# Kernel tuning notes

Hardware: AMD Instinct MI355X
Metric: run time of the kernel (lower is better)

## Reference

```python
import jax, jax.numpy as jnp
import numpy as np

EPS_LN = 1e-6


def _ln(x):
    m = jnp.mean(x, axis=-1, keepdims=True)
    v = jnp.mean((x - m) ** 2, axis=-1, keepdims=True)
    return (x - m) * jax.lax.rsqrt(v + EPS_LN)


def _rope(q, cos, sin):
    # q: [B,S,H,D]; cos/sin: [S, D//2]; rotate interleaved pairs
    q2 = q.reshape(q.shape[:-1] + (-1, 2))
    a, b = q2[..., 0], q2[..., 1]
    c = cos[None, :, None, :]
    s = sin[None, :, None, :]
    return jnp.stack([a * c - b * s, a * s + b * c], axis=-1).reshape(q.shape)


def _attn(q, k, v):
    # q:[B,Sq,H,D] k,v:[B,Sk,H,D] -> [B,Sq,H,D]; flash default scale 1/sqrt(D)
    D = q.shape[-1]
    scores = jnp.einsum('bqhd,bkhd->bhqk', q, k) / jnp.sqrt(jnp.asarray(D, q.dtype))
    p = jax.nn.softmax(scores, axis=-1)
    return jnp.einsum('bhqk,bkhd->bqhd', p, v)


def setup_inputs() -> dict:
    key = jax.random.key(0)
    C, H, S, T, B = 2048, 16, 1024, 256, 4
    Dh = C // H
    F = int(C * 4)
    L, Ly = B * S, B * T
    ks = jax.random.split(key, 24)

    def w(k, shape):
        return (jax.random.normal(k, shape, dtype=jnp.float32) * 0.02)

    # RoPE angle table: positions 0..S-1 with standard inverse frequencies
    inv_freq = 1.0 / (10000.0 ** (np.arange(0, Dh, 2, dtype=np.float32) / Dh))
    freqs = jnp.asarray(np.arange(S, dtype=np.float32)[:, None] * inv_freq[None, :])

    inp = {
        'x': jax.random.normal(ks[0], (L, C), dtype=jnp.float32),
        'y': jax.random.normal(ks[1], (Ly, C), dtype=jnp.float32),
        't': jax.random.normal(ks[2], (L, 6 * C), dtype=jnp.float32),
        'freqs': freqs,
        'scale_shift_table': jax.random.normal(ks[3], (6, C), dtype=jnp.float32) / (C ** 0.5),
        'Wq_s': w(ks[4], (C, C)), 'bq_s': jnp.zeros((C,), jnp.float32),
        'Wk_s': w(ks[5], (C, C)), 'bk_s': jnp.zeros((C,), jnp.float32),
        'Wv_s': w(ks[6], (C, C)), 'bv_s': jnp.zeros((C,), jnp.float32),
        'Wo_s': w(ks[7], (C, C)), 'bo_s': jnp.zeros((C,), jnp.float32),
        'Wq_c': w(ks[8], (C, C)), 'bq_c': jnp.zeros((C,), jnp.float32),
        'Wk_c': w(ks[9], (C, C)), 'bk_c': jnp.zeros((C,), jnp.float32),
        'Wv_c': w(ks[10], (C, C)), 'bv_c': jnp.zeros((C,), jnp.float32),
        'Wo_c': w(ks[11], (C, C)), 'bo_c': jnp.zeros((C,), jnp.float32),
        'W_fc1': w(ks[12], (F, C)), 'b_fc1': jnp.zeros((F,), jnp.float32),
        'W_fc2': w(ks[13], (C, F)), 'b_fc2': jnp.zeros((C,), jnp.float32),
        'seq_len': S,
        'txt_len': T,
    }
    return inp


def reference(x, y, t, freqs, scale_shift_table,
              Wq_s, bq_s, Wk_s, bk_s, Wv_s, bv_s, Wo_s, bo_s,
              Wq_c, bq_c, Wk_c, bk_c, Wv_c, bv_c, Wo_c, bo_c,
              W_fc1, b_fc1, W_fc2, b_fc2, seq_len, txt_len):
    L, C = x.shape
    Dh = 2 * freqs.shape[1]
    H = C // Dh
    B = L // seq_len
    cos, sin = jnp.cos(freqs), jnp.sin(freqs)

    # per-token AdaLN params (B here == total tokens in torch code)
    mods = scale_shift_table[None] + t.reshape(L, 6, C)
    shift_msa, scale_msa, gate_msa, shift_mlp, scale_mlp, gate_mlp = (
        mods[:, i, :] for i in range(6))

    # ---- self attention (AdaLN modulate + RoPE) ----
    xm = _ln(x) * (1.0 + scale_msa) + shift_msa
    q = (xm @ Wq_s.T + bq_s).reshape(B, seq_len, H, Dh)
    k = (xm @ Wk_s.T + bk_s).reshape(B, seq_len, H, Dh)
    v = (xm @ Wv_s.T + bv_s).reshape(B, seq_len, H, Dh)
    q = _rope(q, cos, sin)
    k = _rope(k, cos, sin)
    a = _attn(q, k, v).reshape(L, C)
    x = x + gate_msa * (a @ Wo_s.T + bo_s)

    # ---- cross attention (no norm/modulation/gate, no RoPE) ----
    q = (x @ Wq_c.T + bq_c).reshape(B, seq_len, H, Dh)
    k = (y @ Wk_c.T + bk_c).reshape(B, txt_len, H, Dh)
    v = (y @ Wv_c.T + bv_c).reshape(B, txt_len, H, Dh)
    a = _attn(q, k, v).reshape(L, C)
    x = x + (a @ Wo_c.T + bo_c)

    # ---- MLP with AdaLN modulate + gate ----
    xm = _ln(x) * (1.0 + scale_mlp) + shift_mlp
    h = jax.nn.gelu(xm @ W_fc1.T + b_fc1, approximate=True)
    x = x + gate_mlp * (h @ W_fc2.T + b_fc2)
    return x
```

## Files before the change

kernel.cpp:

```cpp
#include <hip/hip_runtime.h>
#include <stdint.h>

#define C_DIM 2048
#define H_NUM 16
#define DH    128
#define S_LEN 1024
#define T_LEN 256
#define B_SZ  4
#define L_ROWS 4096
#define LY_ROWS 1024
#define F_DIM 8192

typedef __attribute__((ext_vector_type(4))) float f32x4;
typedef __attribute__((ext_vector_type(8))) __bf16 bf16x8;
typedef __attribute__((ext_vector_type(4))) unsigned short us4;
typedef __attribute__((ext_vector_type(8))) unsigned short us8;
typedef unsigned short u16;

__device__ __forceinline__ u16 f2bf(float f) {
  union { float f; uint32_t u; } v; v.f = f;
  uint32_t r = v.u + 0x7FFFu + ((v.u >> 16) & 1u);
  return (u16)(r >> 16);
}
__device__ __forceinline__ float bf2f(u16 h) {
  union { uint32_t u; float f; } v; v.u = ((uint32_t)h) << 16;
  return v.f;
}

typedef __attribute__((address_space(1))) void gvoid;
typedef __attribute__((address_space(3))) void lvoid;
__device__ __forceinline__ void gl_lds16(const void* g, void* l) {
  __builtin_amdgcn_global_load_lds((gvoid*)g, (lvoid*)l, 16, 0, 0);
}

template<int N> __device__ __forceinline__ void wait_vmcnt() {
  if constexpr (N == 0) asm volatile("s_waitcnt vmcnt(0)" ::: "memory");
  else if constexpr (N == 5) asm volatile("s_waitcnt vmcnt(5)" ::: "memory");
  else if constexpr (N == 6) asm volatile("s_waitcnt vmcnt(6)" ::: "memory");
}
__device__ __forceinline__ void barrier_raw() {
  asm volatile("s_barrier" ::: "memory");
}
__device__ __forceinline__ void lgkm0_pin() {
  asm volatile("s_waitcnt lgkmcnt(0)" ::: "memory");
  __builtin_amdgcn_sched_barrier(0);
}

__global__ void k_cvt(const float* __restrict__ src, u16* __restrict__ dst, int n) {
  int i = (blockIdx.x * blockDim.x + threadIdx.x) * 4;
  int stride = gridDim.x * blockDim.x * 4;
  for (; i < n; i += stride) {
    float4 v = *(const float4*)(src + i);
    us4 o;
    o[0] = f2bf(v.x); o[1] = f2bf(v.y); o[2] = f2bf(v.z); o[3] = f2bf(v.w);
    *(us4*)(dst + i) = o;
  }
}

__global__ __launch_bounds__(256)
void k_modln(const float* __restrict__ x, const float* __restrict__ t,
             const float* __restrict__ tab, u16* __restrict__ out,
             int scale_idx, int shift_idx) {
  int row = blockIdx.x;
  int tid = threadIdx.x;
  const float* xr = x + (size_t)row * C_DIM;
  int c0 = tid * 8;
  float4 a = *(const float4*)(xr + c0);
  float4 b = *(const float4*)(xr + c0 + 4);
  float v[8] = {a.x, a.y, a.z, a.w, b.x, b.y, b.z, b.w};
  float s = 0.f, ss = 0.f;
#pragma unroll
  for (int j = 0; j < 8; ++j) { s += v[j]; ss += v[j] * v[j]; }
#pragma unroll
  for (int m = 1; m < 64; m <<= 1) { s += __shfl_xor(s, m); ss += __shfl_xor(ss, m); }
  __shared__ float red[8];
  int wid = tid >> 6;
  if ((tid & 63) == 0) { red[wid * 2] = s; red[wid * 2 + 1] = ss; }
  __syncthreads();
  s  = red[0] + red[2] + red[4] + red[6];
  ss = red[1] + red[3] + red[5] + red[7];
  float mean = s * (1.f / C_DIM);
  float var  = ss * (1.f / C_DIM) - mean * mean;
  float rstd = rsqrtf(var + 1e-6f);
  const float* trow = t + (size_t)row * (6 * C_DIM);
  const float* tsc = trow + scale_idx * C_DIM + c0;
  const float* tsh = trow + shift_idx * C_DIM + c0;
  const float* gsc = tab + scale_idx * C_DIM + c0;
  const float* gsh = tab + shift_idx * C_DIM + c0;
  us8 o;
#pragma unroll
  for (int j = 0; j < 8; ++j) {
    float scv = 1.f + gsc[j] + tsc[j];
    float shv = gsh[j] + tsh[j];
    o[j] = f2bf((v[j] - mean) * rstd * scv + shv);
  }
  *(us8*)(out + (size_t)row * C_DIM + c0) = o;
}

template<int BM, int EPI>
__global__ __launch_bounds__(512, 2)
void k_gemm3(const u16* __restrict__ A, const u16* __restrict__ W,
             const float* __restrict__ bias0, const float* __restrict__ bias1,
             const float* __restrict__ bias2,
             u16* __restrict__ o0, u16* __restrict__ o1, u16* __restrict__ o2,
             int sec_shift, int out_ld,
             float* __restrict__ outF, const float* __restrict__ resid,
             const float* __restrict__ gate_t, const float* __restrict__ gate_tab,
             const float* __restrict__ partial,
             int M, int N, int K, int lda, int ldw, int nbx) {
  constexpr int HTA = (BM / 2) * 64;
  constexpr int HTB = 128 * 64;
  constexpr int ACALLS = BM / 128;
  constexpr int QM = BM / 64;
  constexpr int MFR = BM / 32;
  constexpr int VMN = 4 + ACALLS;
  constexpr int BOFF = 4 * HTA;
  __shared__ __align__(16) u16 lds[BOFF + 4 * HTB];

  int tid = threadIdx.x;
  int nwg = gridDim.x;
  int q8 = nwg >> 3, r8 = nwg & 7;
  int xcd = blockIdx.x & 7, local = blockIdx.x >> 3;
  int wgid = (xcd < r8 ? xcd * (q8 + 1) : r8 * (q8 + 1) + (xcd - r8) * q8) + local;
  int bx = wgid % nbx, by = wgid / nbx;
  int m0 = by * BM, n0 = bx * 256;

  int wid = tid >> 6, lane = tid & 63;
  int wm = wid >> 2, wn = wid & 3;
  int lr = lane & 15, lg = lane >> 4;
  int xorslot = lr & 7;
  int bcol = (wn & 1) * 64;

  int srow = tid >> 3;
  int scol = ((tid ^ (tid >> 3)) & 7) * 8;

  auto stA = [&](int h, int kt2) {
    int pt = kt2 & 1;
    u16* dst = lds + (pt * 2 + h) * HTA + tid * 8;
#pragma unroll
    for (int call = 0; call < ACALLS; ++call) {
      int grow = m0 + h * (BM / 2) + call * 64 + srow;
      gl_lds16(A + (size_t)grow * lda + kt2 * 64 + scol, dst + call * 4096);
    }
  };
  auto stB = [&](int h, int kt2) {
    int pt = kt2 & 1;
    u16* dst = lds + BOFF + (pt * 2 + h) * HTB + tid * 8;
#pragma unroll
    for (int call = 0; call < 2; ++call) {
      int grow = n0 + h * 128 + call * 64 + srow;
      gl_lds16(W + (size_t)grow * ldw + kt2 * 64 + scol, dst + call * 4096);
    }
  };

  f32x4 zero4 = {0.f, 0.f, 0.f, 0.f};
  f32x4 acc[MFR][4];
#pragma unroll
  for (int m = 0; m < MFR; ++m)
#pragma unroll
    for (int n = 0; n < 4; ++n) acc[m][n] = zero4;

  int NT2 = K >> 6;
  stA(0, 0); stA(1, 0); stB(0, 0); stB(1, 0);
  stB(0, 1); stB(1, 1); stA(0, 1);
  wait_vmcnt<VMN>();
  barrier_raw();

  for (int kt = 0; kt < NT2; ++kt) {
    int p = kt & 1;
    const u16* Ah = lds + (p * 2 + wm) * HTA;
    const u16* Bh = lds + BOFF + (p * 2 + (wn >> 1)) * HTB;
    bf16x8 aR[QM][2], bR0[2][2], bR1[2][2];
    bool st1 = (kt + 1) < NT2, st2 = (kt + 2) < NT2;

#pragma unroll
    for (int m = 0; m < QM; ++m) {
      int r = m * 16 + lr;
#pragma unroll
      for (int kk = 0; kk < 2; ++kk)
        aR[m][kk] = *(const bf16x8*)(Ah + r * 64 + ((((kk << 2) | lg) ^ xorslot)) * 8);
    }
#pragma unroll
    for (int n = 0; n < 2; ++n) {
      int r = bcol + n * 16 + lr;
#pragma unroll
      for (int kk = 0; kk < 2; ++kk)
        bR0[n][kk] = *(const bf16x8*)(Bh + r * 64 + ((((kk << 2) | lg) ^ xorslot)) * 8);
    }
    if (st1) stA(1, kt + 1);
    lgkm0_pin();
    __builtin_amdgcn_s_setprio(1);
#pragma unroll
    for (int kk = 0; kk < 2; ++kk)
#pragma unroll
      for (int m = 0; m < QM; ++m)
#pragma unroll
        for (int n = 0; n < 2; ++n)
          acc[m][n] = __builtin_amdgcn_mfma_f32_16x16x32_bf16(aR[m][kk], bR0[n][kk], acc[m][n], 0, 0, 0);
    __builtin_amdgcn_s_setprio(0);
    barrier_raw();

#pragma unroll
    for (int n = 0; n < 2; ++n) {
      int r = bcol + 32 + n * 16 + lr;
#pragma unroll
      for (int kk = 0; kk < 2; ++kk)
        bR1[n][kk] = *(const bf16x8*)(Bh + r * 64 + ((((kk << 2) | lg) ^ xorslot)) * 8);
    }
    lgkm0_pin();
    __builtin_amdgcn_s_setprio(1);
#pragma unroll
    for (int kk = 0; kk < 2; ++kk)
#pragma unroll
      for (int m = 0; m < QM; ++m)
#pragma unroll
        for (int n = 0; n < 2; ++n)
          acc[m][2 + n] = __builtin_amdgcn_mfma_f32_16x16x32_bf16(aR[m][kk], bR1[n][kk], acc[m][2 + n], 0, 0, 0);
    __builtin_amdgcn_s_setprio(0);
    barrier_raw();

#pragma unroll
    for (int m = 0; m < QM; ++m) {
      int r = (BM / 4) + m * 16 + lr;
#pragma unroll
      for (int kk = 0; kk < 2; ++kk)
        aR[m][kk] = *(const bf16x8*)(Ah + r * 64 + ((((kk << 2) | lg) ^ xorslot)) * 8);
    }
    if (st2) { stB(0, kt + 2); stB(1, kt + 2); }
    lgkm0_pin();
    __builtin_amdgcn_s_setprio(1);
#pragma unroll
    for (int kk = 0; kk < 2; ++kk)
#pragma unroll
      for (int m = 0; m < QM; ++m)
#pragma unroll
        for (int n = 0; n < 2; ++n)
          acc[QM + m][2 + n] = __builtin_amdgcn_mfma_f32_16x16x32_bf16(aR[m][kk], bR1[n][kk], acc[QM + m][2 + n], 0, 0, 0);
    __builtin_amdgcn_s_setprio(0);
    barrier_raw();

    if (st2) stA(0, kt + 2);
    __builtin_amdgcn_s_setprio(1);
#pragma unroll
    for (int kk = 0; kk < 2; ++kk)
#pragma unroll
      for (int m = 0; m < QM; ++m)
#pragma unroll
        for (int n = 0; n < 2; ++n)
          acc[QM + m][n] = __builtin_amdgcn_mfma_f32_16x16x32_bf16(aR[m][kk], bR0[n][kk], acc[QM + m][n], 0, 0, 0);
    __builtin_amdgcn_s_setprio(0);
    if (st2) wait_vmcnt<VMN>(); else wait_vmcnt<0>();
    barrier_raw();
  }

#pragma unroll
  for (int mf = 0; mf < MFR; ++mf) {
    int row0 = m0 + wm * (BM / 2) + mf * 16 + lg * 4;
#pragma unroll
    for (int nf = 0; nf < 4; ++nf) {
      int col = n0 + wn * 64 + nf * 16 + lr;
      if constexpr (EPI == 0) {
        int sec = col >> sec_shift;
        const float* bp = sec == 0 ? bias0 : (sec == 1 ? bias1 : bias2);
        u16* op = sec == 0 ? o0 : (sec == 1 ? o1 : o2);
        int cs = col & ((1 << sec_shift) - 1);
        float bv = bp[cs];
#pragma unroll
        for (int r = 0; r < 4; ++r)
          op[(size_t)(row0 + r) * out_ld + cs] = f2bf(acc[mf][nf][r] + bv);
      } else if constexpr (EPI == 1) {
        float bv = bias0[col];
#pragma unroll
        for (int r = 0; r < 4; ++r) {
          float val = acc[mf][nf][r] + bv;
          float x3 = val * val * val;
          float g = 0.5f * val * (1.f + tanhf(0.7978845608f * (val + 0.044715f * x3)));
          o0[(size_t)(row0 + r) * out_ld + col] = f2bf(g);
        }
      } else if constexpr (EPI == 2) {
        float bv = bias0[col];
        float gt = gate_tab[col];
#pragma unroll
        for (int r = 0; r < 4; ++r) {
          int row = row0 + r;
          size_t idx = (size_t)row * N + col;
          float g = gt + gate_t[(size_t)row * (6 * C_DIM) + col];
          float o = resid[idx] + g * (acc[mf][nf][r] + bv);
          outF[idx] = o;
          if (o0) o0[idx] = f2bf(o);
        }
      } else if constexpr (EPI == 3) {
        float bv = bias0[col];
#pragma unroll
        for (int r = 0; r < 4; ++r) {
          size_t idx = (size_t)(row0 + r) * N + col;
          outF[idx] = resid[idx] + (acc[mf][nf][r] + bv);
        }
      } else if constexpr (EPI == 4) {
#pragma unroll
        for (int r = 0; r < 4; ++r)
          outF[(size_t)(row0 + r) * N + col] = acc[mf][nf][r];
      } else {
        float bv = bias0[col];
        float gt = gate_tab[col];
#pragma unroll
        for (int r = 0; r < 4; ++r) {
          int row = row0 + r;
          size_t idx = (size_t)row * N + col;
          float val = acc[mf][nf][r] + partial[idx] + bv;
          float g = gt + gate_t[(size_t)row * (6 * C_DIM) + col];
          outF[idx] = resid[idx] + g * val;
        }
      }
    }
  }
}

__global__ void k_rope(u16* __restrict__ q, u16* __restrict__ k,
                       const float* __restrict__ freqs) {
  int idx = blockIdx.x * blockDim.x + threadIdx.x;
  int total = L_ROWS * C_DIM / 8;
  for (; idx < total; idx += gridDim.x * blockDim.x) {
    int e = idx * 8;
    int row = e >> 11;
    int col = e & (C_DIM - 1);
    int s = row & (S_LEN - 1);
    int i0 = (col & (DH - 1)) >> 1;
    float4 fr = *(const float4*)(freqs + s * (DH / 2) + i0);
    float cs[4], sn[4];
    float fv[4] = {fr.x, fr.y, fr.z, fr.w};
#pragma unroll
    for (int j = 0; j < 4; ++j) sincosf(fv[j], &sn[j], &cs[j]);
    us8 qa = *(us8*)(q + e);
    us8 ka = *(us8*)(k + e);
#pragma unroll
    for (int p = 0; p < 4; ++p) {
      float a = bf2f(qa[2 * p]), b = bf2f(qa[2 * p + 1]);
      qa[2 * p]     = f2bf(a * cs[p] - b * sn[p]);
      qa[2 * p + 1] = f2bf(a * sn[p] + b * cs[p]);
      float a2 = bf2f(ka[2 * p]), b2 = bf2f(ka[2 * p + 1]);
      ka[2 * p]     = f2bf(a2 * cs[p] - b2 * sn[p]);
      ka[2 * p + 1] = f2bf(a2 * sn[p] + b2 * cs[p]);
    }
    *(us8*)(q + e) = qa;
    *(us8*)(k + e) = ka;
  }
}

__global__ void k_transpose_v(const u16* __restrict__ v, u16* __restrict__ vt, int Lkv) {
  __shared__ u16 tile[32][33];
  int bh = blockIdx.x, b = bh >> 4, h = bh & 15;
  int k0 = blockIdx.y * 32, d0 = blockIdx.z * 32;
  int tx = threadIdx.x, ty = threadIdx.y;
  const u16* src = v + (size_t)(b * Lkv) * C_DIM + h * DH;
#pragma unroll
  for (int j = 0; j < 32; j += 8)
    tile[ty + j][tx] = src[(size_t)(k0 + ty + j) * C_DIM + d0 + tx];
  __syncthreads();
  u16* dst = vt + (size_t)bh * DH * Lkv;
#pragma unroll
  for (int j = 0; j < 32; j += 8)
    dst[(size_t)(d0 + ty + j) * Lkv + k0 + tx] = tile[tx][ty + j];
}

__global__ __launch_bounds__(256)
void k_flash(const u16* __restrict__ Q, const u16* __restrict__ K,
             const u16* __restrict__ Vt, u16* __restrict__ O,
             int Lq, int Lkv, float scale) {
  __shared__ __align__(16) u16 lK[64 * 128];
  __shared__ __align__(16) u16 lV[128 * 64];
  __shared__ __align__(16) u16 lP[4][16 * 72];
  int bh = blockIdx.x, b = bh >> 4, h = bh & 15;
  int tid = threadIdx.x, wid = tid >> 6, lane = tid & 63;
  int lr = lane & 15, lg = lane >> 4;
  int q0 = blockIdx.y * 64 + wid * 16;
  const u16* Qb = Q + ((size_t)(b * Lq) + q0) * C_DIM + h * DH;
  const u16* Kb = K + (size_t)(b * Lkv) * C_DIM + h * DH;
  const u16* Vb = Vt + (size_t)bh * DH * Lkv;

  bf16x8 qf[4];
#pragma unroll
  for (int ks = 0; ks < 4; ++ks)
    qf[ks] = *(const bf16x8*)(Qb + (size_t)lr * C_DIM + ks * 32 + lg * 8);

  f32x4 zero4 = {0.f, 0.f, 0.f, 0.f};
  f32x4 o[8];
#pragma unroll
  for (int n = 0; n < 8; ++n) o[n] = zero4;
  float mrow[4] = {-3.0e38f, -3.0e38f, -3.0e38f, -3.0e38f};
  float lrow[4] = {0.f, 0.f, 0.f, 0.f};

  int nsteps = Lkv >> 6;
  for (int kt = 0; kt < nsteps; ++kt) {
#pragma unroll
    for (int i = 0; i < 4; ++i) {
      int flat = i * 4096 + tid * 16;
      int key = flat >> 8, inner = flat & 255;
      int ksrc = inner ^ ((key & 7) << 4);
      gl_lds16((const char*)Kb + ((size_t)(kt * 64 + key) * C_DIM) * 2 + ksrc, (char*)lK + flat);
      int d = flat >> 7, keyb = flat & 127;
      int vsrc = keyb ^ ((d & 7) << 4);
      gl_lds16((const char*)Vb + ((size_t)d * Lkv) * 2 + kt * 128 + vsrc, (char*)lV + flat);
    }
    __syncthreads();

    f32x4 sc[4];
#pragma unroll
    for (int c = 0; c < 4; ++c) sc[c] = zero4;
#pragma unroll
    for (int c = 0; c < 4; ++c) {
      int key = c * 16 + lr;
#pragma unroll
      for (int ks = 0; ks < 4; ++ks) {
        int off = (ks * 64 + lg * 16) ^ ((key & 7) << 4);
        bf16x8 kf = *(const bf16x8*)((const char*)lK + key * 256 + off);
        sc[c] = __builtin_amdgcn_mfma_f32_16x16x32_bf16(qf[ks], kf, sc[c], 0, 0, 0);
      }
    }
#pragma unroll
    for (int r = 0; r < 4; ++r) {
      float s0 = sc[0][r] * scale, s1 = sc[1][r] * scale;
      float s2 = sc[2][r] * scale, s3 = sc[3][r] * scale;
      float mx = fmaxf(fmaxf(s0, s1), fmaxf(s2, s3));
#pragma unroll
      for (int m = 1; m < 16; m <<= 1) mx = fmaxf(mx, __shfl_xor(mx, m));
      float mnew = fmaxf(mrow[r], mx);
      float alpha = exp2f((mrow[r] - mnew) * 1.44269504f);
      mrow[r] = mnew;
      float p0 = exp2f((s0 - mnew) * 1.44269504f);
      float p1 = exp2f((s1 - mnew) * 1.44269504f);
      float p2 = exp2f((s2 - mnew) * 1.44269504f);
      float p3 = exp2f((s3 - mnew) * 1.44269504f);
      float psum = p0 + p1 + p2 + p3;
#pragma unroll
      for (int m = 1; m < 16; m <<= 1) psum += __shfl_xor(psum, m);
      lrow[r] = lrow[r] * alpha + psum;
#pragma unroll
      for (int n = 0; n < 8; ++n) o[n][r] *= alpha;
      u16* pr = lP[wid] + (4 * lg + r) * 72;
      pr[lr]      = f2bf(p0);
      pr[16 + lr] = f2bf(p1);
      pr[32 + lr] = f2bf(p2);
      pr[48 + lr] = f2bf(p3);
    }
    asm volatile("s_waitcnt lgkmcnt(0)" ::: "memory");
    __builtin_amdgcn_sched_barrier(0);
#pragma unroll
    for (int half = 0; half < 2; ++half) {
      bf16x8 pf = *(const bf16x8*)(lP[wid] + lr * 72 + half * 32 + lg * 8);
#pragma unroll
      for (int n = 0; n < 8; ++n) {
        int d = n * 16 + lr;
        int off = (half * 64 + lg * 16) ^ ((d & 7) << 4);
        bf16x8 vf = *(const bf16x8*)((const char*)lV + d * 128 + off);
        o[n] = __builtin_amdgcn_mfma_f32_16x16x32_bf16(pf, vf, o[n], 0, 0, 0);
      }
    }
    __syncthreads();
  }

  u16* Ob = O + ((size_t)(b * Lq) + q0) * C_DIM + h * DH;
#pragma unroll
  for (int n = 0; n < 8; ++n) {
    int d = n * 16 + lr;
#pragma unroll
    for (int r = 0; r < 4; ++r) {
      int qr = 4 * lg + r;
      Ob[(size_t)qr * C_DIM + d] = f2bf(o[n][r] / lrow[r]);
    }
  }
}

extern "C" void kernel_launch(void* const* d_in, const int* in_sizes, int n_in,
                              void* d_out, int out_size, void* d_ws, size_t ws_size,
                              hipStream_t stream) {
  const float* x     = (const float*)d_in[0];
  const float* y     = (const float*)d_in[1];
  const float* t     = (const float*)d_in[2];
  const float* freqs = (const float*)d_in[3];
  const float* tab   = (const float*)d_in[4];
  const float* Wq_s = (const float*)d_in[5];
  const float* bq_s = (const float*)d_in[6];
  const float* Wk_s = (const float*)d_in[7];
  const float* bk_s = (const float*)d_in[8];
  const float* Wv_s = (const float*)d_in[9];
  const float* bv_s = (const float*)d_in[10];
  const float* Wo_s = (const float*)d_in[11];
  const float* bo_s = (const float*)d_in[12];
  const float* Wq_c = (const float*)d_in[13];
  const float* bq_c = (const float*)d_in[14];
  const float* Wk_c = (const float*)d_in[15];
  const float* bk_c = (const float*)d_in[16];
  const float* Wv_c = (const float*)d_in[17];
  const float* bv_c = (const float*)d_in[18];
  const float* Wo_c = (const float*)d_in[19];
  const float* bo_c = (const float*)d_in[20];
  const float* W_fc1 = (const float*)d_in[21];
  const float* b_fc1 = (const float*)d_in[22];
  const float* W_fc2 = (const float*)d_in[23];
  const float* b_fc2 = (const float*)d_in[24];

  const size_t SZ_CC  = (size_t)C_DIM * C_DIM * 2;
  const size_t SZ_FC  = (size_t)F_DIM * C_DIM * 2;
  const size_t SZ_LC  = (size_t)L_ROWS * C_DIM * 2;
  const size_t SZ_YC  = (size_t)LY_ROWS * C_DIM * 2;
  char* ws = (char*)d_ws;
  size_t off = 0;
  u16* wq_s = (u16*)(ws + off); off += SZ_CC;
  u16* wk_s = (u16*)(ws + off); off += SZ_CC;
  u16* wv_s = (u16*)(ws + off); off += SZ_CC;
  u16* wo_s = (u16*)(ws + off); off += SZ_CC;
  u16* wq_c = (u16*)(ws + off); off += SZ_CC;
  u16* wk_c = (u16*)(ws + off); off += SZ_CC;
  u16* wv_c = (u16*)(ws + off); off += SZ_CC;
  u16* wo_c = (u16*)(ws + off); off += SZ_CC;
  u16* wfc1 = (u16*)(ws + off); off += SZ_FC;
  u16* wfc2 = (u16*)(ws + off); off += SZ_FC;
  u16* ybf  = (u16*)(ws + off); off += SZ_YC;
  u16* xm   = (u16*)(ws + off); off += SZ_LC;
  u16* qb   = (u16*)(ws + off); off += SZ_LC;
  u16* kb   = (u16*)(ws + off); off += SZ_LC;
  u16* vb   = (u16*)(ws + off); off += SZ_LC;
  u16* ao   = (u16*)(ws + off); off += SZ_LC;
  u16* hbuf = qb;
  float* x1 = (float*)(ws + off); off += (size_t)L_ROWS * C_DIM * 4;
  u16* x1bf = (u16*)(ws + off); off += SZ_LC;
  u16* kc   = (u16*)(ws + off); off += SZ_YC;
  u16* vc   = (u16*)(ws + off); off += SZ_YC;
  u16* vt   = (u16*)(ws + off); off += SZ_LC;
  u16* vtc  = (u16*)(ws + off); off += SZ_YC;
  float* part = (float*)x1bf;
  if (ws_size < off) return;

  auto cvt = [&](const float* s, u16* d, int n) {
    int blocks = (n / 4 + 255) / 256; if (blocks > 4096) blocks = 4096;
    k_cvt<<<blocks, 256, 0, stream>>>(s, d, n);
  };
  cvt(Wq_s, wq_s, C_DIM * C_DIM);
  cvt(Wk_s, wk_s, C_DIM * C_DIM);
  cvt(Wv_s, wv_s, C_DIM * C_DIM);
  cvt(Wo_s, wo_s, C_DIM * C_DIM);
  cvt(Wq_c, wq_c, C_DIM * C_DIM);
  cvt(Wk_c, wk_c, C_DIM * C_DIM);
  cvt(Wv_c, wv_c, C_DIM * C_DIM);
  cvt(Wo_c, wo_c, C_DIM * C_DIM);
  cvt(W_fc1, wfc1, F_DIM * C_DIM);
  cvt(W_fc2, wfc2, F_DIM * C_DIM);
  cvt(y, ybf, LY_ROWS * C_DIM);

  const float ascale = 0.08838834764831845f;

  k_modln<<<L_ROWS, 256, 0, stream>>>(x, t, tab, xm, 1, 0);
  k_gemm3<128, 0><<<32 * 24, 512, 0, stream>>>(
      xm, wq_s, bq_s, bk_s, bv_s, qb, kb, vb, 11, C_DIM,
      nullptr, nullptr, nullptr, nullptr, nullptr, L_ROWS, 6144, C_DIM, C_DIM, C_DIM, 24);
  k_rope<<<2048, 256, 0, stream>>>(qb, kb, freqs);
  k_transpose_v<<<dim3(B_SZ * H_NUM, S_LEN / 32, DH / 32), dim3(32, 8), 0, stream>>>(vb, vt, S_LEN);
  k_flash<<<dim3(B_SZ * H_NUM, S_LEN / 64), 256, 0, stream>>>(qb, kb, vt, ao, S_LEN, S_LEN, ascale);
  k_gemm3<128, 2><<<32 * 8, 512, 0, stream>>>(
      ao, wo_s, bo_s, nullptr, nullptr, x1bf, nullptr, nullptr, 30, C_DIM,
      x1, x, t + 2 * C_DIM, tab + 2 * C_DIM, nullptr, L_ROWS, C_DIM, C_DIM, C_DIM, C_DIM, 8);
  k_gemm3<128, 0><<<32 * 8, 512, 0, stream>>>(
      x1bf, wq_c, bq_c, nullptr, nullptr, qb, nullptr, nullptr, 30, C_DIM,
      nullptr, nullptr, nullptr, nullptr, nullptr, L_ROWS, C_DIM, C_DIM, C_DIM, C_DIM, 8);
  k_gemm3<128, 0><<<8 * 16, 512, 0, stream>>>(
      ybf, wk_c, bk_c, bv_c, bv_c, kc, vc, vc, 11, C_DIM,
      nullptr, nullptr, nullptr, nullptr, nullptr, LY_ROWS, 4096, C_DIM, C_DIM, C_DIM, 16);
  k_transpose_v<<<dim3(B_SZ * H_NUM, T_LEN / 32, DH / 32), dim3(32, 8), 0, stream>>>(vc, vtc, T_LEN);
  k_flash<<<dim3(B_SZ * H_NUM, S_LEN / 64), 256, 0, stream>>>(qb, kc, vtc, ao, S_LEN, T_LEN, ascale);
  k_gemm3<128, 3><<<32 * 8, 512, 0, stream>>>(
      ao, wo_c, bo_c, nullptr, nullptr, nullptr, nullptr, nullptr, 30, C_DIM,
      x1, x1, nullptr, nullptr, nullptr, L_ROWS, C_DIM, C_DIM, C_DIM, C_DIM, 8);
  k_modln<<<L_ROWS, 256, 0, stream>>>(x1, t, tab, xm, 4, 3);
  k_gemm3<256, 1><<<16 * 32, 512, 0, stream>>>(
      xm, wfc1, b_fc1, nullptr, nullptr, hbuf, nullptr, nullptr, 30, F_DIM,
      nullptr, nullptr, nullptr, nullptr, nullptr, L_ROWS, F_DIM, C_DIM, C_DIM, C_DIM, 32);
  k_gemm3<128, 4><<<32 * 8, 512, 0, stream>>>(
      hbuf, wfc2, nullptr, nullptr, nullptr, nullptr, nullptr, nullptr, 30, C_DIM,
      part, nullptr, nullptr, nullptr, nullptr, L_ROWS, C_DIM, F_DIM / 2, F_DIM, F_DIM, 8);
  k_gemm3<128, 5><<<32 * 8, 512, 0, stream>>>(
      hbuf + F_DIM / 2, wfc2 + F_DIM / 2, b_fc2, nullptr, nullptr, nullptr, nullptr, nullptr, 30, C_DIM,
      (float*)d_out, x1, t + 5 * C_DIM, tab + 5 * C_DIM, part,
      L_ROWS, C_DIM, F_DIM / 2, F_DIM, F_DIM, 8);
}
```

Measured before the change: 917.9 us.

## Restructure GEMM k-loop to two barriers per tile with separate A-half registers

The GEMM main loop now loads both B column halves up front and keeps separate registers for the low and high A row halves. This cuts the per-k-tile barriers from four to two and drops the explicit lgkmcnt(0) waits, leaving the compiler to insert LDS waits. All next-stage global-to-LDS prefetches are issued together after the first barrier. FC1 also moves from a 256-row tile to a 128-row tile with twice the blocks. The extra fragment registers raise pressure under the 2-blocks-per-CU launch bound, and removing the explicit waits risks less overlap between LDS reads and MFMA issue.

```diff
diff --git a/kernel.cpp b/kernel.cpp
--- a/kernel.cpp
+++ b/kernel.cpp
@@ -41,10 +41,7 @@
 __device__ __forceinline__ void barrier_raw() {
   asm volatile("s_barrier" ::: "memory");
 }
-__device__ __forceinline__ void lgkm0_pin() {
-  asm volatile("s_waitcnt lgkmcnt(0)" ::: "memory");
-  __builtin_amdgcn_sched_barrier(0);
-}
+__device__ __forceinline__ void sb0() { __builtin_amdgcn_sched_barrier(0); }
 
 __global__ void k_cvt(const float* __restrict__ src, u16* __restrict__ dst, int n) {
   int i = (blockIdx.x * blockDim.x + threadIdx.x) * 4;
@@ -99,7 +96,7 @@
 
 template<int BM, int EPI>
 __global__ __launch_bounds__(512, 2)
-void k_gemm3(const u16* __restrict__ A, const u16* __restrict__ W,
+void k_gemm4(const u16* __restrict__ A, const u16* __restrict__ W,
              const float* __restrict__ bias0, const float* __restrict__ bias1,
              const float* __restrict__ bias2,
              u16* __restrict__ o0, u16* __restrict__ o1, u16* __restrict__ o2,
@@ -170,7 +167,7 @@
     int p = kt & 1;
     const u16* Ah = lds + (p * 2 + wm) * HTA;
     const u16* Bh = lds + BOFF + (p * 2 + (wn >> 1)) * HTB;
-    bf16x8 aR[QM][2], bR0[2][2], bR1[2][2];
+    bf16x8 aL[QM][2], aH[QM][2], b0[2][2], b1[2][2];
     bool st1 = (kt + 1) < NT2, st2 = (kt + 2) < NT2;
 
 #pragma unroll
@@ -178,17 +175,24 @@
       int r = m * 16 + lr;
 #pragma unroll
       for (int kk = 0; kk < 2; ++kk)
-        aR[m][kk] = *(const bf16x8*)(Ah + r * 64 + ((((kk << 2) | lg) ^ xorslot)) * 8);
+        aL[m][kk] = *(const bf16x8*)(Ah + r * 64 + (((kk << 2) | lg) ^ xorslot) * 8);
     }
 #pragma unroll
     for (int n = 0; n < 2; ++n) {
       int r = bcol + n * 16 + lr;
 #pragma unroll
       for (int kk = 0; kk < 2; ++kk)
-        bR0[n][kk] = *(const bf16x8*)(Bh + r * 64 + ((((kk << 2) | lg) ^ xorslot)) * 8);
+        b0[n][kk] = *(const bf16x8*)(Bh + r * 64 + (((kk << 2) | lg) ^ xorslot) * 8);
     }
     if (st1) stA(1, kt + 1);
-    lgkm0_pin();
+#pragma unroll
+    for (int n = 0; n < 2; ++n) {
+      int r = bcol + 32 + n * 16 + lr;
+#pragma unroll
+      for (int kk = 0; kk < 2; ++kk)
+        b1[n][kk] = *(const bf16x8*)(Bh + r * 64 + (((kk << 2) | lg) ^ xorslot) * 8);
+    }
+    sb0();
     __builtin_amdgcn_s_setprio(1);
 #pragma unroll
     for (int kk = 0; kk < 2; ++kk)
@@ -196,18 +200,29 @@
       for (int m = 0; m < QM; ++m)
 #pragma unroll
         for (int n = 0; n < 2; ++n)
-          acc[m][n] = __builtin_amdgcn_mfma_f32_16x16x32_bf16(aR[m][kk], bR0[n][kk], acc[m][n], 0, 0, 0);
+          acc[m][n] = __builtin_amdgcn_mfma_f32_16x16x32_bf16(aL[m][kk], b0[n][kk], acc[m][n], 0, 0, 0);
+    __builtin_amdgcn_s_setprio(0);
+    sb0();
+#pragma unroll
+    for (int m = 0; m < QM; ++m) {
+      int r = (BM / 4) + m * 16 + lr;
+#pragma unroll
+      for (int kk = 0; kk < 2; ++kk)
+        aH[m][kk] = *(const bf16x8*)(Ah + r * 64 + (((kk << 2) | lg) ^ xorslot) * 8);
+    }
+    sb0();
+    __builtin_amdgcn_s_setprio(1);
+#pragma unroll
+    for (int kk = 0; kk < 2; ++kk)
+#pragma unroll
+      for (int m = 0; m < QM; ++m)
+#pragma unroll
+        for (int n = 0; n < 2; ++n)
+          acc[m][2 + n] = __builtin_amdgcn_mfma_f32_16x16x32_bf16(aL[m][kk], b1[n][kk], acc[m][2 + n], 0, 0, 0);
     __builtin_amdgcn_s_setprio(0);
     barrier_raw();
-
-#pragma unroll
-    for (int n = 0; n < 2; ++n) {
-      int r = bcol + 32 + n * 16 + lr;
-#pragma unroll
-      for (int kk = 0; kk < 2; ++kk)
-        bR1[n][kk] = *(const bf16x8*)(Bh + r * 64 + ((((kk << 2) | lg) ^ xorslot)) * 8);
-    }
-    lgkm0_pin();
+    if (st2) { stB(0, kt + 2); stB(1, kt + 2); stA(0, kt + 2); }
+    sb0();
     __builtin_amdgcn_s_setprio(1);
 #pragma unroll
     for (int kk = 0; kk < 2; ++kk)
@@ -215,39 +230,14 @@
       for (int m = 0; m < QM; ++m)
 #pragma unroll
         for (int n = 0; n < 2; ++n)
-          acc[m][2 + n] = __builtin_amdgcn_mfma_f32_16x16x32_bf16(aR[m][kk], bR1[n][kk], acc[m][2 + n], 0, 0, 0);
-    __builtin_amdgcn_s_setprio(0);
-    barrier_raw();
-
-#pragma unroll
-    for (int m = 0; m < QM; ++m) {
-      int r = (BM / 4) + m * 16 + lr;
-#pragma unroll
-      for (int kk = 0; kk < 2; ++kk)
-        aR[m][kk] = *(const bf16x8*)(Ah + r * 64 + ((((kk << 2) | lg) ^ xorslot)) * 8);
-    }
-    if (st2) { stB(0, kt + 2); stB(1, kt + 2); }
-    lgkm0_pin();
-    __builtin_amdgcn_s_setprio(1);
+          acc[QM + m][2 + n] = __builtin_amdgcn_mfma_f32_16x16x32_bf16(aH[m][kk], b1[n][kk], acc[QM + m][2 + n], 0, 0, 0);
 #pragma unroll
     for (int kk = 0; kk < 2; ++kk)
 #pragma unroll
       for (int m = 0; m < QM; ++m)
 #pragma unroll
         for (int n = 0; n < 2; ++n)
-          acc[QM + m][2 + n] = __builtin_amdgcn_mfma_f32_16x16x32_bf16(aR[m][kk], bR1[n][kk], acc[QM + m][2 + n], 0, 0, 0);
-    __builtin_amdgcn_s_setprio(0);
-    barrier_raw();
-
-    if (st2) stA(0, kt + 2);
-    __builtin_amdgcn_s_setprio(1);
-#pragma unroll
-    for (int kk = 0; kk < 2; ++kk)
-#pragma unroll
-      for (int m = 0; m < QM; ++m)
-#pragma unroll
-        for (int n = 0; n < 2; ++n)
-          acc[QM + m][n] = __builtin_amdgcn_mfma_f32_16x16x32_bf16(aR[m][kk], bR0[n][kk], acc[QM + m][n], 0, 0, 0);
+          acc[QM + m][n] = __builtin_amdgcn_mfma_f32_16x16x32_bf16(aH[m][kk], b0[n][kk], acc[QM + m][n], 0, 0, 0);
     __builtin_amdgcn_s_setprio(0);
     if (st2) wait_vmcnt<VMN>(); else wait_vmcnt<0>();
     barrier_raw();
@@ -551,34 +541,34 @@
   const float ascale = 0.08838834764831845f;
 
   k_modln<<<L_ROWS, 256, 0, stream>>>(x, t, tab, xm, 1, 0);
-  k_gemm3<128, 0><<<32 * 24, 512, 0, stream>>>(
+  k_gemm4<128, 0><<<32 * 24, 512, 0, stream>>>(
       xm, wq_s, bq_s, bk_s, bv_s, qb, kb, vb, 11, C_DIM,
       nullptr, nullptr, nullptr, nullptr, nullptr, L_ROWS, 6144, C_DIM, C_DIM, C_DIM, 24);
   k_rope<<<2048, 256, 0, stream>>>(qb, kb, freqs);
   k_transpose_v<<<dim3(B_SZ * H_NUM, S_LEN / 32, DH / 32), dim3(32, 8), 0, stream>>>(vb, vt, S_LEN);
   k_flash<<<dim3(B_SZ * H_NUM, S_LEN / 64), 256, 0, stream>>>(qb, kb, vt, ao, S_LEN, S_LEN, ascale);
-  k_gemm3<128, 2><<<32 * 8, 512, 0, stream>>>(
+  k_gemm4<128, 2><<<32 * 8, 512, 0, stream>>>(
       ao, wo_s, bo_s, nullptr, nullptr, x1bf, nullptr, nullptr, 30, C_DIM,
       x1, x, t + 2 * C_DIM, tab + 2 * C_DIM, nullptr, L_ROWS, C_DIM, C_DIM, C_DIM, C_DIM, 8);
-  k_gemm3<128, 0><<<32 * 8, 512, 0, stream>>>(
+  k_gemm4<128, 0><<<32 * 8, 512, 0, stream>>>(
       x1bf, wq_c, bq_c, nullptr, nullptr, qb, nullptr, nullptr, 30, C_DIM,
       nullptr, nullptr, nullptr, nullptr, nullptr, L_ROWS, C_DIM, C_DIM, C_DIM, C_DIM, 8);
-  k_gemm3<128, 0><<<8 * 16, 512, 0, stream>>>(
+  k_gemm4<128, 0><<<8 * 16, 512, 0, stream>>>(
       ybf, wk_c, bk_c, bv_c, bv_c, kc, vc, vc, 11, C_DIM,
       nullptr, nullptr, nullptr, nullptr, nullptr, LY_ROWS, 4096, C_DIM, C_DIM, C_DIM, 16);
   k_transpose_v<<<dim3(B_SZ * H_NUM, T_LEN / 32, DH / 32), dim3(32, 8), 0, stream>>>(vc, vtc, T_LEN);
   k_flash<<<dim3(B_SZ * H_NUM, S_LEN / 64), 256, 0, stream>>>(qb, kc, vtc, ao, S_LEN, T_LEN, ascale);
-  k_gemm3<128, 3><<<32 * 8, 512, 0, stream>>>(
+  k_gemm4<128, 3><<<32 * 8, 512, 0, stream>>>(
       ao, wo_c, bo_c, nullptr, nullptr, nullptr, nullptr, nullptr, 30, C_DIM,
       x1, x1, nullptr, nullptr, nullptr, L_ROWS, C_DIM, C_DIM, C_DIM, C_DIM, 8);
   k_modln<<<L_ROWS, 256, 0, stream>>>(x1, t, tab, xm, 4, 3);
-  k_gemm3<256, 1><<<16 * 32, 512, 0, stream>>>(
+  k_gemm4<128, 1><<<32 * 32, 512, 0, stream>>>(
       xm, wfc1, b_fc1, nullptr, nullptr, hbuf, nullptr, nullptr, 30, F_DIM,
       nullptr, nullptr, nullptr, nullptr, nullptr, L_ROWS, F_DIM, C_DIM, C_DIM, C_DIM, 32);
-  k_gemm3<128, 4><<<32 * 8, 512, 0, stream>>>(
+  k_gemm4<128, 4><<<32 * 8, 512, 0, stream>>>(
       hbuf, wfc2, nullptr, nullptr, nullptr, nullptr, nullptr, nullptr, 30, C_DIM,
       part, nullptr, nullptr, nullptr, nullptr, L_ROWS, C_DIM, F_DIM / 2, F_DIM, F_DIM, 8);
-  k_gemm3<128, 5><<<32 * 8, 512, 0, stream>>>(
+  k_gemm4<128, 5><<<32 * 8, 512, 0, stream>>>(
       hbuf + F_DIM / 2, wfc2 + F_DIM / 2, b_fc2, nullptr, nullptr, nullptr, nullptr, nullptr, 30, C_DIM,
       (float*)d_out, x1, t + 5 * C_DIM, tab + 5 * C_DIM, part,
       L_ROWS, C_DIM, F_DIM / 2, F_DIM, F_DIM, 8);
```

Measured after the change: 955.6 us. 1.04x slower.
